# Kernel optimization log

Measured on AMD Instinct MI355X. Metric: run time of the kernel, lower is better.

The kernel has to match this reference:

```python
import jax, jax.numpy as jnp
import numpy as np

NUM_ITERATIONS = 3


def squash(s, axis):
    # s: capsule vectors; squash along `axis` (capsule dim)
    mag_sq = jnp.sum(s * s, axis=axis, keepdims=True)
    mag = jnp.sqrt(mag_sq)
    return mag_sq / (1.0 + mag_sq) * (s / mag)


def setup_inputs() -> dict:
    key = jax.random.key(0)
    k1, k2 = jax.random.split(key)
    B, IN_SIZE, I = 256, 8, 1152   # batch, in_size, in_node_num
    N, O = 10, 16                  # num_node, node_size
    x = jax.random.normal(k1, (B, IN_SIZE, I), dtype=jnp.float32)
    W = jax.random.normal(k2, (1, I, N, O, IN_SIZE), dtype=jnp.float32)
    return {"x": x, "W": W}


def reference(x, W):
    # x: (B, in_size, I); W: (1, I, N, O, in_size)
    B = x.shape[0]
    I, N = W.shape[1], W.shape[2]
    xt = jnp.swapaxes(x, 1, 2)  # (B, I, in_size)
    # u_hat[b,i,n,o] = sum_k (0.03*W[0,i,n,o,k]) * x[b,i,k]
    u_hat = jnp.einsum('inok,bik->bino', W[0] * 0.03, xt)  # (B, I, N, O)
    b_ij = jnp.zeros((I, N), dtype=x.dtype)
    v_j = None
    for _ in range(NUM_ITERATIONS):
        c_ij = jax.nn.softmax(b_ij, axis=1)              # softmax over num_node
        s_j = jnp.einsum('in,bino->bno', c_ij, u_hat)    # (B, N, O)
        v_j = squash(s_j, axis=-1)                       # squash over node_size
        # agreement: u_hat . v_j, averaged over batch
        u_vj = jnp.einsum('bino,bno->bin', u_hat, v_j).mean(axis=0)  # (I, N)
        b_ij = b_ij + u_vj
    return v_j[:, :, :, None]  # (B, N, O, 1) == v_j.squeeze(1) in torch
```

## Files before the change

kernel.cpp:

```cpp
#include <hip/hip_runtime.h>

#define B_   256
#define I_   1152
#define N_   10
#define P_   9216
#define NO_  160
#define BIJS 12
#define NBLK 1280

typedef unsigned short u16;
typedef short s8v __attribute__((ext_vector_type(8)));
typedef float f4v __attribute__((ext_vector_type(4)));

__device__ inline float bf2f(u16 u){
  unsigned v = ((unsigned)u) << 16; float f; __builtin_memcpy(&f, &v, 4); return f;
}
__device__ inline u16 f2bf(float f){
  unsigned b; __builtin_memcpy(&b, &f, 4);
  b += 0x7fffu + ((b >> 16) & 1u);
  return (u16)(b >> 16);
}
__device__ inline float ald1(const float* p){
  unsigned u = __hip_atomic_load((const unsigned*)p,
      __ATOMIC_RELAXED, __HIP_MEMORY_SCOPE_AGENT);
  float f; __builtin_memcpy(&f, &u, 4); return f;
}
__device__ inline void ast1(float* p, float v){
  unsigned u; __builtin_memcpy(&u, &v, 4);
  __hip_atomic_store((unsigned*)p, u, __ATOMIC_RELAXED, __HIP_MEMORY_SCOPE_AGENT);
}

#define CIX(j) ((j) + (((j) >> 3) << 1))

__global__ __launch_bounds__(128) void k_prep(
    const float* __restrict__ x, const float* __restrict__ W,
    u16* __restrict__ xbp, u16* __restrict__ xpb, u16* __restrict__ Wt,
    float* __restrict__ bij, float* __restrict__ sA, int* __restrict__ bar){
  __shared__ union { u16 w[8][136]; float t[32][68]; } sm;
  int t = threadIdx.x, u = blockIdx.x;
  if (u < 1440){
    int q = u/9, ch = u - q*9;
    int n = q >> 4, o = q & 15;
    int i = ch*128 + t;
    const float* src = W + (size_t)i*1280 + n*128 + o*8;
    float4 a = *reinterpret_cast<const float4*>(src);
    float4 b = *reinterpret_cast<const float4*>(src + 4);
    float vv[8] = {a.x,a.y,a.z,a.w,b.x,b.y,b.z,b.w};
    #pragma unroll
    for (int k = 0; k < 8; ++k) sm.w[k][t] = f2bf(vv[k] * 0.03f);
    __syncthreads();
    int k = t >> 4, seg = t & 15;
    uint4 val = *reinterpret_cast<const uint4*>(&sm.w[k][seg*8]);
    *reinterpret_cast<uint4*>(Wt + (size_t)q*P_ + (size_t)k*I_ + ch*128 + seg*8) = val;
  } else if (u < 2592){
    int v = u - 1440;
    int tb = v/144, tp = v - tb*144;
    int b0 = tb*32, p0 = tp*64;
    #pragma unroll
    for (int pass = 0; pass < 2; ++pass){
      int vt = t + (pass << 7);
      int r = vt >> 3, c8 = (vt & 7)*8;
      const float* sp = x + (size_t)(b0 + r)*P_ + p0 + c8;
      float4 a = *reinterpret_cast<const float4*>(sp);
      float4 b = *reinterpret_cast<const float4*>(sp + 4);
      *reinterpret_cast<float4*>(&sm.t[r][c8]) = a;
      *reinterpret_cast<float4*>(&sm.t[r][c8+4]) = b;
      uint4 pk;
      pk.x = (unsigned)f2bf(a.x) | ((unsigned)f2bf(a.y) << 16);
      pk.y = (unsigned)f2bf(a.z) | ((unsigned)f2bf(a.w) << 16);
      pk.z = (unsigned)f2bf(b.x) | ((unsigned)f2bf(b.y) << 16);
      pk.w = (unsigned)f2bf(b.z) | ((unsigned)f2bf(b.w) << 16);
      *reinterpret_cast<uint4*>(xbp + (size_t)(b0 + r)*P_ + p0 + c8) = pk;
    }
    __syncthreads();
    #pragma unroll
    for (int pass = 0; pass < 2; ++pass){
      int vt = t + (pass << 7);
      int pc = vt >> 2, rb = (vt & 3)*8;
      uint4 pk;
      pk.x = (unsigned)f2bf(sm.t[rb+0][pc]) | ((unsigned)f2bf(sm.t[rb+1][pc]) << 16);
      pk.y = (unsigned)f2bf(sm.t[rb+2][pc]) | ((unsigned)f2bf(sm.t[rb+3][pc]) << 16);
      pk.z = (unsigned)f2bf(sm.t[rb+4][pc]) | ((unsigned)f2bf(sm.t[rb+5][pc]) << 16);
      pk.w = (unsigned)f2bf(sm.t[rb+6][pc]) | ((unsigned)f2bf(sm.t[rb+7][pc]) << 16);
      *reinterpret_cast<uint4*>(xpb + (size_t)(p0 + pc)*B_ + b0 + rb) = pk;
    }
  } else if (u < 2700){
    bij[(u - 2592)*128 + t] = 0.f;
  } else if (u < 3020){
    sA[(u - 2700)*128 + t] = 0.f;
  } else {
    for (int z = t; z < 4128; z += 128) bar[z] = 0;
  }
}

__device__ inline void gbar(int* bar, int bid, int ph){
  __syncthreads();
  if (threadIdx.x == 0){
    int li = bid & 63;
    if (__hip_atomic_fetch_add(bar + li*32, 1, __ATOMIC_RELAXED,
                               __HIP_MEMORY_SCOPE_AGENT) == ph*20 - 1){
      if (__hip_atomic_fetch_add(bar + 4096, 1, __ATOMIC_RELAXED,
                                 __HIP_MEMORY_SCOPE_AGENT) == ph*64 - 1){
        #pragma unroll
        for (int z = 0; z < 64; ++z)
          __hip_atomic_store(bar + 2048 + z*32, ph, __ATOMIC_RELAXED,
                             __HIP_MEMORY_SCOPE_AGENT);
      }
    }
    while (__hip_atomic_load(bar + 2048 + li*32, __ATOMIC_RELAXED,
                             __HIP_MEMORY_SCOPE_AGENT) < ph)
      __builtin_amdgcn_s_sleep(4);
  }
  __syncthreads();
}

union LdsU {
  struct { float c[720]; u16 Bt[16][592]; } S;
  u16 vl[32][264];
};

__device__ inline void phase_C(int t, int bid,
    const float* __restrict__ bij, float* __restrict__ cT)
{
  if (bid < 9){
    int j = bid*128 + t;
    const float* br = bij + (size_t)j*BIJS;
    f4v a; f4v b4; float2 c2;
    asm volatile(
      "global_load_dwordx4 %0, %3, off sc0 sc1\n\t"
      "global_load_dwordx4 %1, %3, off offset:16 sc0 sc1\n\t"
      "global_load_dwordx2 %2, %3, off offset:32 sc0 sc1\n\t"
      "s_waitcnt vmcnt(0)"
      : "=&v"(a), "=&v"(b4), "=&v"(c2)
      : "v"(br) : "memory");
    float l[10] = {a[0],a[1],a[2],a[3],b4[0],b4[1],b4[2],b4[3],c2.x,c2.y};
    float mx = l[0];
    #pragma unroll
    for (int k = 1; k < 10; ++k) mx = fmaxf(mx, l[k]);
    float e[10]; float se = 0.f;
    #pragma unroll
    for (int k = 0; k < 10; ++k){ e[k] = __expf(l[k]-mx); se += e[k]; }
    float inv = 1.0f / se;
    #pragma unroll
    for (int k = 0; k < 10; ++k) ast1(&cT[k*I_ + j], e[k]*inv);
  }
}

__device__ inline void phase_S(int t, int bid,
    const u16* __restrict__ xbp, const u16* __restrict__ Wt,
    const float* __restrict__ cT, float* __restrict__ s_cur,
    float* __restrict__ s_zero, LdsU* lds)
{
  int kc = (bid & 7)*2 + ((bid >> 3) & 1);
  int g2 = bid >> 4;
  int n = g2 % 10, bx2 = g2 / 10;
  if (s_zero && t < 32) ast1(&s_zero[bid*32 + t], 0.f);
  int i0 = (kc & 1)*576;

  const float* cp = cT + (size_t)n*I_ + i0;
  {
    float4 v = *reinterpret_cast<const float4*>(cp + 4*t);
    int d = CIX(4*t);
    lds->S.c[d] = v.x; lds->S.c[d+1] = v.y; lds->S.c[d+2] = v.z; lds->S.c[d+3] = v.w;
    if (t < 16){
      float4 w = *reinterpret_cast<const float4*>(cp + 512 + 4*t);
      int d2 = CIX(512 + 4*t);
      lds->S.c[d2] = w.x; lds->S.c[d2+1] = w.y; lds->S.c[d2+2] = w.z; lds->S.c[d2+3] = w.w;
    }
  }
  __syncthreads();

  #pragma unroll
  for (int s9 = 0; s9 < 9; ++s9){
    int uu = t + s9*128;
    int r = uu / 72, m = uu - r*72;
    uint4 w = *reinterpret_cast<const uint4*>(Wt + (size_t)(n*16 + r)*P_ + kc*576 + m*8);
    const float* cc = &lds->S.c[10*m];
    float2 ca = *reinterpret_cast<const float2*>(cc);
    float2 cb = *reinterpret_cast<const float2*>(cc + 2);
    float2 cd = *reinterpret_cast<const float2*>(cc + 4);
    float2 ce = *reinterpret_cast<const float2*>(cc + 6);
    uint4 rr;
    rr.x = (unsigned)f2bf(bf2f(w.x & 0xffff)*ca.x) | ((unsigned)f2bf(bf2f(w.x >> 16)*ca.y) << 16);
    rr.y = (unsigned)f2bf(bf2f(w.y & 0xffff)*cb.x) | ((unsigned)f2bf(bf2f(w.y >> 16)*cb.y) << 16);
    rr.z = (unsigned)f2bf(bf2f(w.z & 0xffff)*cd.x) | ((unsigned)f2bf(bf2f(w.z >> 16)*cd.y) << 16);
    rr.w = (unsigned)f2bf(bf2f(w.w & 0xffff)*ce.x) | ((unsigned)f2bf(bf2f(w.w >> 16)*ce.y) << 16);
    *reinterpret_cast<uint4*>(&lds->S.Bt[r][m*8]) = rr;
  }
  __syncthreads();

  int wid = t >> 6, l = t & 63, lo = l & 15, quad = l >> 4;
  int b0 = bx2*32 + wid*16;
  const s8v* ap = reinterpret_cast<const s8v*>(xbp + (size_t)(b0 + lo)*P_ + kc*576 + quad*8);
  f4v acc0 = {0.f,0.f,0.f,0.f}, acc1 = {0.f,0.f,0.f,0.f};
  #pragma unroll
  for (int s = 0; s < 9; ++s){
    s8v a0 = ap[8*s];
    s8v b0v = *reinterpret_cast<const s8v*>(&lds->S.Bt[lo][quad*8 + 64*s]);
    s8v a1 = ap[8*s + 4];
    s8v b1v = *reinterpret_cast<const s8v*>(&lds->S.Bt[lo][quad*8 + 64*s + 32]);
    acc0 = __builtin_amdgcn_mfma_f32_16x16x32_bf16(a0, b0v, acc0, 0, 0, 0);
    acc1 = __builtin_amdgcn_mfma_f32_16x16x32_bf16(a1, b1v, acc1, 0, 0, 0);
  }
  f4v acc = acc0 + acc1;
  int r0 = quad << 2;
  #pragma unroll
  for (int r = 0; r < 4; ++r)
    atomicAdd(&s_cur[(size_t)(b0 + r0 + r)*NO_ + n*16 + lo], acc[r]);
}

__device__ inline void phase_G(int t, int bid,
    const u16* __restrict__ xpb, const float* __restrict__ s,
    const u16* __restrict__ Wt, float* __restrict__ bij, LdsU* lds)
{
  int qp = bid >> 8;
  #pragma unroll
  for (int h = 0; h < 2; ++h){
    int b = t + (h << 7);
    #pragma unroll
    for (int nn = 0; nn < 2; ++nn){
      const float* sr = s + (size_t)b*NO_ + (qp*2 + nn)*16;
      float4 s0 = *reinterpret_cast<const float4*>(sr);
      float4 s1 = *reinterpret_cast<const float4*>(sr + 4);
      float4 s2 = *reinterpret_cast<const float4*>(sr + 8);
      float4 s3 = *reinterpret_cast<const float4*>(sr + 12);
      float sq = s0.x*s0.x+s0.y*s0.y+s0.z*s0.z+s0.w*s0.w
               + s1.x*s1.x+s1.y*s1.y+s1.z*s1.z+s1.w*s1.w
               + s2.x*s2.x+s2.y*s2.y+s2.z*s2.z+s2.w*s2.w
               + s3.x*s3.x+s3.y*s3.y+s3.z*s3.z+s3.w*s3.w;
      float scale = sqrtf(sq) / (1.0f + sq);
      float sv[16] = {s0.x,s0.y,s0.z,s0.w,s1.x,s1.y,s1.z,s1.w,
                      s2.x,s2.y,s2.z,s2.w,s3.x,s3.y,s3.z,s3.w};
      #pragma unroll
      for (int o = 0; o < 16; ++o)
        lds->vl[nn*16 + o][b] = f2bf(sv[o] * scale);
    }
  }
  __syncthreads();

  int wv = t >> 6, l = t & 63, lo = l & 15, quad = l >> 4;
  int idx = (139*(bid & 255)) & 255;
  for (int u = idx*2 + wv; u < 576; u += 512){
    int p0 = u << 4;
    const s8v* ap = reinterpret_cast<const s8v*>(xpb + (size_t)(p0 + lo)*B_ + quad*8);
    f4v acc0 = {0.f,0.f,0.f,0.f}, acc1 = {0.f,0.f,0.f,0.f};
    #pragma unroll
    for (int st = 0; st < 8; ++st){
      s8v a  = ap[4*st];
      s8v b0 = *reinterpret_cast<const s8v*>(&lds->vl[lo]     [st*32 + quad*8]);
      s8v b1 = *reinterpret_cast<const s8v*>(&lds->vl[16 + lo][st*32 + quad*8]);
      acc0 = __builtin_amdgcn_mfma_f32_16x16x32_bf16(a, b0, acc0, 0, 0, 0);
      acc1 = __builtin_amdgcn_mfma_f32_16x16x32_bf16(a, b1, acc1, 0, 0, 0);
    }
    int ib = p0 % 1152;
    #pragma unroll
    for (int sb = 0; sb < 2; ++sb){
      f4v acc = sb ? acc1 : acc0;
      int n = qp*2 + sb;
      const u16* wp = Wt + (size_t)(n*16 + lo)*P_ + p0 + (quad << 2);
      ushort4 w4 = *reinterpret_cast<const ushort4*>(wp);
      float v0 = acc[0]*bf2f(w4.x), v1 = acc[1]*bf2f(w4.y);
      float v2 = acc[2]*bf2f(w4.z), v3 = acc[3]*bf2f(w4.w);
      #pragma unroll
      for (int m = 8; m >= 1; m >>= 1){
        v0 += __shfl_xor(v0, m, 16);
        v1 += __shfl_xor(v1, m, 16);
        v2 += __shfl_xor(v2, m, 16);
        v3 += __shfl_xor(v3, m, 16);
      }
      if (lo == 0){
        int i = ib + (quad << 2);
        atomicAdd(&bij[(size_t)(i+0)*BIJS + n], v0 * (1.f/256.f));
        atomicAdd(&bij[(size_t)(i+1)*BIJS + n], v1 * (1.f/256.f));
        atomicAdd(&bij[(size_t)(i+2)*BIJS + n], v2 * (1.f/256.f));
        atomicAdd(&bij[(size_t)(i+3)*BIJS + n], v3 * (1.f/256.f));
      }
    }
  }
}

__global__ __launch_bounds__(128, 3) void k_route(
    const u16* __restrict__ xbp, const u16* __restrict__ xpb,
    const u16* __restrict__ Wt, float* __restrict__ bij,
    float* __restrict__ cTa, float* __restrict__ cTb,
    float* __restrict__ sA, float* __restrict__ sB,
    float* __restrict__ out, int* __restrict__ bar)
{
  __shared__ LdsU lds;
  int t = threadIdx.x, bid = blockIdx.x;

  {
    int kc = (bid & 7)*2 + ((bid >> 3) & 1);
    int g2 = bid >> 4;
    int n = g2 % 10, bx2 = g2 / 10;
    if (t < 32) ast1(&sB[bid*32 + t], 0.f);
    int wid = t >> 6, l = t & 63, lo = l & 15, quad = l >> 4;
    int b0 = bx2*32 + wid*16;
    const s8v* ap = reinterpret_cast<const s8v*>(xbp + (size_t)(b0 + lo)*P_ + kc*576 + quad*8);
    const s8v* bp = reinterpret_cast<const s8v*>(Wt  + (size_t)(n*16 + lo)*P_ + kc*576 + quad*8);
    f4v acc0 = {0.f,0.f,0.f,0.f}, acc1 = {0.f,0.f,0.f,0.f};
    #pragma unroll
    for (int s = 0; s < 9; ++s){
      acc0 = __builtin_amdgcn_mfma_f32_16x16x32_bf16(ap[8*s],     bp[8*s],     acc0, 0, 0, 0);
      acc1 = __builtin_amdgcn_mfma_f32_16x16x32_bf16(ap[8*s + 4], bp[8*s + 4], acc1, 0, 0, 0);
    }
    f4v acc = acc0 + acc1;
    int r0 = quad << 2;
    #pragma unroll
    for (int r = 0; r < 4; ++r)
      atomicAdd(&sA[(size_t)(b0 + r0 + r)*NO_ + n*16 + lo], acc[r] * 0.1f);
  }
  gbar(bar, bid, 1);

  phase_G(t, bid, xpb, sA, Wt, bij, &lds);
  gbar(bar, bid, 2);

  phase_C(t, bid, bij, cTa);
  gbar(bar, bid, 3);

  phase_S(t, bid, xbp, Wt, cTa, sB, sA, &lds);
  gbar(bar, bid, 4);

  phase_G(t, bid, xpb, sB, Wt, bij, &lds);
  gbar(bar, bid, 5);

  phase_C(t, bid, bij, cTb);
  gbar(bar, bid, 6);

  phase_S(t, bid, xbp, Wt, cTb, sA, nullptr, &lds);
  gbar(bar, bid, 7);

  if (bid < 320){
    int o = t & 15, rl = t >> 4;
    int rowid = bid*8 + rl;
    int b = rowid / 10, n = rowid - b*10;
    size_t idx = (size_t)b*NO_ + n*16 + o;
    float sv = ald1(&sA[idx]);
    float sq = sv * sv;
    #pragma unroll
    for (int m = 8; m >= 1; m >>= 1) sq += __shfl_xor(sq, m, 16);
    out[idx] = sv * sqrtf(sq) / (1.0f + sq);
  }
}

extern "C" void kernel_launch(void* const* d_in, const int* in_sizes, int n_in,
                              void* d_out, int out_size, void* d_ws, size_t ws_size,
                              hipStream_t stream){
  (void)in_sizes; (void)n_in; (void)out_size; (void)ws_size;
  const float* x = (const float*)d_in[0];
  const float* W = (const float*)d_in[1];
  float* out = (float*)d_out;

  float* sA  = (float*)d_ws;
  float* sB  = sA + 40960;
  float* bij = sB + 40960;
  float* cTa = bij + 13824;
  float* cTb = cTa + 11520;
  u16* xbp = (u16*)(cTb + 11520);
  u16* xpb = xbp + 2359296;
  u16* Wt  = xpb + 2359296;
  int* bar = (int*)(Wt + 1474560);

  k_prep <<<3021, 128, 0, stream>>>(x, W, xbp, xpb, Wt, bij, sA, bar);
  k_route<<<NBLK, 128, 0, stream>>>(xbp, xpb, Wt, bij, cTa, cTb, sA, sB, out, bar);
}
```

Before: 141.3 us.

## Fuse agreement and softmax phases, halve grid, drop two grid barriers

Reworks the persistent routing kernel. Squash/v computation is done once by ten dedicated blocks into a global bf16 buffer, signalled through a counter instead of being recomputed in every block. The agreement reduction is repartitioned so each of 72 blocks owns 16 input capsules, accumulates b_ij in LDS and registers, and applies the softmax locally. This removes the global b_ij atomics and the separate softmax phase plus its grid barriers. The grid is halved to 640 blocks with twice the work per block in the S phases, which trades fewer barrier participants for less parallelism in the G phase, where only 72 blocks do the matmul work.

```diff
diff --git a/kernel.cpp b/kernel.cpp
--- a/kernel.cpp
+++ b/kernel.cpp
@@ -5,8 +5,7 @@
 #define N_   10
 #define P_   9216
 #define NO_  160
-#define BIJS 12
-#define NBLK 1280
+#define NBLK 640
 
 typedef unsigned short u16;
 typedef short s8v __attribute__((ext_vector_type(8)));
@@ -20,6 +19,12 @@
   b += 0x7fffu + ((b >> 16) & 1u);
   return (u16)(b >> 16);
 }
+__device__ inline void ald2(const float* p, float& a, float& b){
+  unsigned long long q = __hip_atomic_load((const unsigned long long*)p,
+      __ATOMIC_RELAXED, __HIP_MEMORY_SCOPE_AGENT);
+  unsigned lo = (unsigned)q, hi = (unsigned)(q >> 32);
+  __builtin_memcpy(&a, &lo, 4); __builtin_memcpy(&b, &hi, 4);
+}
 __device__ inline float ald1(const float* p){
   unsigned u = __hip_atomic_load((const unsigned*)p,
       __ATOMIC_RELAXED, __HIP_MEMORY_SCOPE_AGENT);
@@ -29,13 +34,16 @@
   unsigned u; __builtin_memcpy(&u, &v, 4);
   __hip_atomic_store((unsigned*)p, u, __ATOMIC_RELAXED, __HIP_MEMORY_SCOPE_AGENT);
 }
+__device__ inline void astu(unsigned* p, unsigned v){
+  __hip_atomic_store(p, v, __ATOMIC_RELAXED, __HIP_MEMORY_SCOPE_AGENT);
+}
 
 #define CIX(j) ((j) + (((j) >> 3) << 1))
 
 __global__ __launch_bounds__(128) void k_prep(
     const float* __restrict__ x, const float* __restrict__ W,
     u16* __restrict__ xbp, u16* __restrict__ xpb, u16* __restrict__ Wt,
-    float* __restrict__ bij, float* __restrict__ sA, int* __restrict__ bar){
+    float* __restrict__ sA, int* __restrict__ bar){
   __shared__ union { u16 w[8][136]; float t[32][68]; } sm;
   int t = threadIdx.x, u = blockIdx.x;
   if (u < 1440){
@@ -84,10 +92,8 @@
       pk.w = (unsigned)f2bf(sm.t[rb+6][pc]) | ((unsigned)f2bf(sm.t[rb+7][pc]) << 16);
       *reinterpret_cast<uint4*>(xpb + (size_t)(p0 + pc)*B_ + b0 + rb) = pk;
     }
-  } else if (u < 2700){
-    bij[(u - 2592)*128 + t] = 0.f;
-  } else if (u < 3020){
-    sA[(u - 2700)*128 + t] = 0.f;
+  } else if (u < 2912){
+    sA[(u - 2592)*128 + t] = 0.f;
   } else {
     for (int z = t; z < 4128; z += 128) bar[z] = 0;
   }
@@ -98,7 +104,7 @@
   if (threadIdx.x == 0){
     int li = bid & 63;
     if (__hip_atomic_fetch_add(bar + li*32, 1, __ATOMIC_RELAXED,
-                               __HIP_MEMORY_SCOPE_AGENT) == ph*20 - 1){
+                               __HIP_MEMORY_SCOPE_AGENT) == ph*10 - 1){
       if (__hip_atomic_fetch_add(bar + 4096, 1, __ATOMIC_RELAXED,
                                  __HIP_MEMORY_SCOPE_AGENT) == ph*64 - 1){
         #pragma unroll
@@ -116,33 +122,107 @@
 
 union LdsU {
   struct { float c[720]; u16 Bt[16][592]; } S;
-  u16 vl[32][264];
+  struct { float bijL[16][10]; } G;
 };
 
-__device__ inline void phase_C(int t, int bid,
-    const float* __restrict__ bij, float* __restrict__ cT)
+__device__ inline void phase_VG(int t, int bid,
+    const u16* __restrict__ xpb, const u16* __restrict__ Wt,
+    const float* __restrict__ s, u16* __restrict__ vbt,
+    float* __restrict__ cT, int* __restrict__ bar, int vthr,
+    float* bijr, LdsU* lds)
 {
-  if (bid < 9){
-    int j = bid*128 + t;
-    const float* br = bij + (size_t)j*BIJS;
-    f4v a; f4v b4; float2 c2;
-    asm volatile(
-      "global_load_dwordx4 %0, %3, off sc0 sc1\n\t"
-      "global_load_dwordx4 %1, %3, off offset:16 sc0 sc1\n\t"
-      "global_load_dwordx2 %2, %3, off offset:32 sc0 sc1\n\t"
-      "s_waitcnt vmcnt(0)"
-      : "=&v"(a), "=&v"(b4), "=&v"(c2)
-      : "v"(br) : "memory");
-    float l[10] = {a[0],a[1],a[2],a[3],b4[0],b4[1],b4[2],b4[3],c2.x,c2.y};
-    float mx = l[0];
-    #pragma unroll
-    for (int k = 1; k < 10; ++k) mx = fmaxf(mx, l[k]);
-    float e[10]; float se = 0.f;
-    #pragma unroll
-    for (int k = 0; k < 10; ++k){ e[k] = __expf(l[k]-mx); se += e[k]; }
-    float inv = 1.0f / se;
-    #pragma unroll
-    for (int k = 0; k < 10; ++k) ast1(&cT[k*I_ + j], e[k]*inv);
+  if (bid >= 72 && bid < 82){
+    int n = bid - 72, bp = t, b0 = bp*2;
+    const float* s0p = s + (size_t)b0*NO_ + n*16;
+    const float* s1p = s0p + NO_;
+    float v0[16], v1[16];
+    #pragma unroll
+    for (int k = 0; k < 8; ++k){
+      ald2(s0p + 2*k, v0[2*k], v0[2*k+1]);
+      ald2(s1p + 2*k, v1[2*k], v1[2*k+1]);
+    }
+    float sq0 = 0.f, sq1 = 0.f;
+    #pragma unroll
+    for (int o = 0; o < 16; ++o){ sq0 += v0[o]*v0[o]; sq1 += v1[o]*v1[o]; }
+    float sc0 = sqrtf(sq0)/(1.0f + sq0), sc1 = sqrtf(sq1)/(1.0f + sq1);
+    unsigned* vb32 = reinterpret_cast<unsigned*>(vbt);
+    #pragma unroll
+    for (int o = 0; o < 16; ++o){
+      unsigned pk = (unsigned)f2bf(v0[o]*sc0) | ((unsigned)f2bf(v1[o]*sc1) << 16);
+      astu(&vb32[(n*16 + o)*128 + bp], pk);
+    }
+    __syncthreads();
+    if (t == 0)
+      __hip_atomic_fetch_add(bar + 4100, 1, __ATOMIC_RELAXED, __HIP_MEMORY_SCOPE_AGENT);
+  } else if (bid < 72){
+    for (int z = t; z < 160; z += 128)
+      reinterpret_cast<float*>(lds->G.bijL)[z] = 0.f;
+    if (t == 0){
+      while (__hip_atomic_load(bar + 4100, __ATOMIC_RELAXED,
+                               __HIP_MEMORY_SCOPE_AGENT) < vthr)
+        __builtin_amdgcn_s_sleep(2);
+    }
+    __syncthreads();
+    int wv = t >> 6, l = t & 63, lo = l & 15, quad = l >> 4;
+    int i0 = bid*16;
+    #pragma unroll
+    for (int kk = 0; kk < 4; ++kk){
+      int k = wv*4 + kk;
+      int p0 = k*1152 + i0;
+      const s8v* ap = reinterpret_cast<const s8v*>(xpb + (size_t)(p0 + lo)*B_ + quad*8);
+      #pragma unroll
+      for (int np = 0; np < 5; ++np){
+        int n0 = np*2;
+        const s8v* b0p = reinterpret_cast<const s8v*>(vbt + (size_t)(n0*16 + lo)*B_ + quad*8);
+        const s8v* b1p = reinterpret_cast<const s8v*>(vbt + (size_t)((n0+1)*16 + lo)*B_ + quad*8);
+        f4v acc0 = {0.f,0.f,0.f,0.f}, acc1 = {0.f,0.f,0.f,0.f};
+        #pragma unroll
+        for (int st = 0; st < 8; ++st){
+          s8v a = ap[4*st];
+          acc0 = __builtin_amdgcn_mfma_f32_16x16x32_bf16(a, b0p[4*st], acc0, 0, 0, 0);
+          acc1 = __builtin_amdgcn_mfma_f32_16x16x32_bf16(a, b1p[4*st], acc1, 0, 0, 0);
+        }
+        #pragma unroll
+        for (int sb = 0; sb < 2; ++sb){
+          f4v acc = sb ? acc1 : acc0;
+          int n = n0 + sb;
+          ushort4 w4 = *reinterpret_cast<const ushort4*>(
+              Wt + (size_t)(n*16 + lo)*P_ + p0 + quad*4);
+          float v0 = acc[0]*bf2f(w4.x), v1 = acc[1]*bf2f(w4.y);
+          float v2 = acc[2]*bf2f(w4.z), v3 = acc[3]*bf2f(w4.w);
+          #pragma unroll
+          for (int m = 8; m >= 1; m >>= 1){
+            v0 += __shfl_xor(v0, m, 16);
+            v1 += __shfl_xor(v1, m, 16);
+            v2 += __shfl_xor(v2, m, 16);
+            v3 += __shfl_xor(v3, m, 16);
+          }
+          if (lo == 0){
+            int r0 = quad*4;
+            atomicAdd(&lds->G.bijL[r0+0][n], v0 * (1.f/256.f));
+            atomicAdd(&lds->G.bijL[r0+1][n], v1 * (1.f/256.f));
+            atomicAdd(&lds->G.bijL[r0+2][n], v2 * (1.f/256.f));
+            atomicAdd(&lds->G.bijL[r0+3][n], v3 * (1.f/256.f));
+          }
+        }
+      }
+    }
+    __syncthreads();
+    if (t < 16){
+      float e[10]; float mx = -1e30f;
+      #pragma unroll
+      for (int j = 0; j < 10; ++j){
+        bijr[j] += lds->G.bijL[t][j];
+        mx = fmaxf(mx, bijr[j]);
+      }
+      float se = 0.f;
+      #pragma unroll
+      for (int j = 0; j < 10; ++j){ e[j] = __expf(bijr[j] - mx); se += e[j]; }
+      float inv = 1.0f / se;
+      #pragma unroll
+      for (int j = 0; j < 10; ++j)
+        ast1(&cT[(size_t)j*I_ + i0 + t], e[j] * inv);
+    }
   }
 }
 
@@ -151,56 +231,57 @@
     const float* __restrict__ cT, float* __restrict__ s_cur,
     float* __restrict__ s_zero, LdsU* lds)
 {
-  int kc = (bid & 7)*2 + ((bid >> 3) & 1);
-  int g2 = bid >> 4;
-  int n = g2 % 10, bx2 = g2 / 10;
-  if (s_zero && t < 32) ast1(&s_zero[bid*32 + t], 0.f);
-  int i0 = (kc & 1)*576;
-
-  const float* cp = cT + (size_t)n*I_ + i0;
-  {
-    float4 v = *reinterpret_cast<const float4*>(cp + 4*t);
-    int d = CIX(4*t);
-    lds->S.c[d] = v.x; lds->S.c[d+1] = v.y; lds->S.c[d+2] = v.z; lds->S.c[d+3] = v.w;
-    if (t < 16){
-      float4 w = *reinterpret_cast<const float4*>(cp + 512 + 4*t);
-      int d2 = CIX(512 + 4*t);
-      lds->S.c[d2] = w.x; lds->S.c[d2+1] = w.y; lds->S.c[d2+2] = w.z; lds->S.c[d2+3] = w.w;
-    }
-  }
-  __syncthreads();
-
-  #pragma unroll
-  for (int s9 = 0; s9 < 9; ++s9){
-    int uu = t + s9*128;
-    int r = uu / 72, m = uu - r*72;
-    uint4 w = *reinterpret_cast<const uint4*>(Wt + (size_t)(n*16 + r)*P_ + kc*576 + m*8);
-    const float* cc = &lds->S.c[10*m];
-    float2 ca = *reinterpret_cast<const float2*>(cc);
-    float2 cb = *reinterpret_cast<const float2*>(cc + 2);
-    float2 cd = *reinterpret_cast<const float2*>(cc + 4);
-    float2 ce = *reinterpret_cast<const float2*>(cc + 6);
-    uint4 rr;
-    rr.x = (unsigned)f2bf(bf2f(w.x & 0xffff)*ca.x) | ((unsigned)f2bf(bf2f(w.x >> 16)*ca.y) << 16);
-    rr.y = (unsigned)f2bf(bf2f(w.y & 0xffff)*cb.x) | ((unsigned)f2bf(bf2f(w.y >> 16)*cb.y) << 16);
-    rr.z = (unsigned)f2bf(bf2f(w.z & 0xffff)*cd.x) | ((unsigned)f2bf(bf2f(w.z >> 16)*cd.y) << 16);
-    rr.w = (unsigned)f2bf(bf2f(w.w & 0xffff)*ce.x) | ((unsigned)f2bf(bf2f(w.w >> 16)*ce.y) << 16);
-    *reinterpret_cast<uint4*>(&lds->S.Bt[r][m*8]) = rr;
-  }
-  __syncthreads();
-
+  int kc = bid & 7, rest = bid >> 3;
+  int n = rest % 10, bx2 = rest / 10;
+  if (s_zero && t < 64) ast1(&s_zero[bid*64 + t], 0.f);
   int wid = t >> 6, l = t & 63, lo = l & 15, quad = l >> 4;
   int b0 = bx2*32 + wid*16;
-  const s8v* ap = reinterpret_cast<const s8v*>(xbp + (size_t)(b0 + lo)*P_ + kc*576 + quad*8);
   f4v acc0 = {0.f,0.f,0.f,0.f}, acc1 = {0.f,0.f,0.f,0.f};
+
   #pragma unroll
-  for (int s = 0; s < 9; ++s){
-    s8v a0 = ap[8*s];
-    s8v b0v = *reinterpret_cast<const s8v*>(&lds->S.Bt[lo][quad*8 + 64*s]);
-    s8v a1 = ap[8*s + 4];
-    s8v b1v = *reinterpret_cast<const s8v*>(&lds->S.Bt[lo][quad*8 + 64*s + 32]);
-    acc0 = __builtin_amdgcn_mfma_f32_16x16x32_bf16(a0, b0v, acc0, 0, 0, 0);
-    acc1 = __builtin_amdgcn_mfma_f32_16x16x32_bf16(a1, b1v, acc1, 0, 0, 0);
+  for (int h2 = 0; h2 < 2; ++h2){
+    int off = kc*1152 + h2*576;
+    const float* cp = cT + (size_t)n*I_ + h2*576;
+    __syncthreads();
+    {
+      float4 v = *reinterpret_cast<const float4*>(cp + 4*t);
+      int d = CIX(4*t);
+      lds->S.c[d] = v.x; lds->S.c[d+1] = v.y; lds->S.c[d+2] = v.z; lds->S.c[d+3] = v.w;
+      if (t < 16){
+        float4 w = *reinterpret_cast<const float4*>(cp + 512 + 4*t);
+        int d2 = CIX(512 + 4*t);
+        lds->S.c[d2] = w.x; lds->S.c[d2+1] = w.y; lds->S.c[d2+2] = w.z; lds->S.c[d2+3] = w.w;
+      }
+    }
+    __syncthreads();
+    #pragma unroll
+    for (int s9 = 0; s9 < 9; ++s9){
+      int uu = t + s9*128;
+      int r = uu / 72, m = uu - r*72;
+      uint4 w = *reinterpret_cast<const uint4*>(Wt + (size_t)(n*16 + r)*P_ + off + m*8);
+      const float* cc = &lds->S.c[10*m];
+      float2 ca = *reinterpret_cast<const float2*>(cc);
+      float2 cb = *reinterpret_cast<const float2*>(cc + 2);
+      float2 cd = *reinterpret_cast<const float2*>(cc + 4);
+      float2 ce = *reinterpret_cast<const float2*>(cc + 6);
+      uint4 rr;
+      rr.x = (unsigned)f2bf(bf2f(w.x & 0xffff)*ca.x) | ((unsigned)f2bf(bf2f(w.x >> 16)*ca.y) << 16);
+      rr.y = (unsigned)f2bf(bf2f(w.y & 0xffff)*cb.x) | ((unsigned)f2bf(bf2f(w.y >> 16)*cb.y) << 16);
+      rr.z = (unsigned)f2bf(bf2f(w.z & 0xffff)*cd.x) | ((unsigned)f2bf(bf2f(w.z >> 16)*cd.y) << 16);
+      rr.w = (unsigned)f2bf(bf2f(w.w & 0xffff)*ce.x) | ((unsigned)f2bf(bf2f(w.w >> 16)*ce.y) << 16);
+      *reinterpret_cast<uint4*>(&lds->S.Bt[r][m*8]) = rr;
+    }
+    __syncthreads();
+    const s8v* ap = reinterpret_cast<const s8v*>(xbp + (size_t)(b0 + lo)*P_ + off + quad*8);
+    #pragma unroll
+    for (int s = 0; s < 9; ++s){
+      s8v a0 = ap[8*s];
+      s8v b0v = *reinterpret_cast<const s8v*>(&lds->S.Bt[lo][quad*8 + 64*s]);
+      s8v a1 = ap[8*s + 4];
+      s8v b1v = *reinterpret_cast<const s8v*>(&lds->S.Bt[lo][quad*8 + 64*s + 32]);
+      acc0 = __builtin_amdgcn_mfma_f32_16x16x32_bf16(a0, b0v, acc0, 0, 0, 0);
+      acc1 = __builtin_amdgcn_mfma_f32_16x16x32_bf16(a1, b1v, acc1, 0, 0, 0);
+    }
   }
   f4v acc = acc0 + acc1;
   int r0 = quad << 2;
@@ -209,98 +290,31 @@
     atomicAdd(&s_cur[(size_t)(b0 + r0 + r)*NO_ + n*16 + lo], acc[r]);
 }
 
-__device__ inline void phase_G(int t, int bid,
-    const u16* __restrict__ xpb, const float* __restrict__ s,
-    const u16* __restrict__ Wt, float* __restrict__ bij, LdsU* lds)
-{
-  int qp = bid >> 8;
-  #pragma unroll
-  for (int h = 0; h < 2; ++h){
-    int b = t + (h << 7);
-    #pragma unroll
-    for (int nn = 0; nn < 2; ++nn){
-      const float* sr = s + (size_t)b*NO_ + (qp*2 + nn)*16;
-      float4 s0 = *reinterpret_cast<const float4*>(sr);
-      float4 s1 = *reinterpret_cast<const float4*>(sr + 4);
-      float4 s2 = *reinterpret_cast<const float4*>(sr + 8);
-      float4 s3 = *reinterpret_cast<const float4*>(sr + 12);
-      float sq = s0.x*s0.x+s0.y*s0.y+s0.z*s0.z+s0.w*s0.w
-               + s1.x*s1.x+s1.y*s1.y+s1.z*s1.z+s1.w*s1.w
-               + s2.x*s2.x+s2.y*s2.y+s2.z*s2.z+s2.w*s2.w
-               + s3.x*s3.x+s3.y*s3.y+s3.z*s3.z+s3.w*s3.w;
-      float scale = sqrtf(sq) / (1.0f + sq);
-      float sv[16] = {s0.x,s0.y,s0.z,s0.w,s1.x,s1.y,s1.z,s1.w,
-                      s2.x,s2.y,s2.z,s2.w,s3.x,s3.y,s3.z,s3.w};
-      #pragma unroll
-      for (int o = 0; o < 16; ++o)
-        lds->vl[nn*16 + o][b] = f2bf(sv[o] * scale);
-    }
-  }
-  __syncthreads();
-
-  int wv = t >> 6, l = t & 63, lo = l & 15, quad = l >> 4;
-  int idx = (139*(bid & 255)) & 255;
-  for (int u = idx*2 + wv; u < 576; u += 512){
-    int p0 = u << 4;
-    const s8v* ap = reinterpret_cast<const s8v*>(xpb + (size_t)(p0 + lo)*B_ + quad*8);
-    f4v acc0 = {0.f,0.f,0.f,0.f}, acc1 = {0.f,0.f,0.f,0.f};
-    #pragma unroll
-    for (int st = 0; st < 8; ++st){
-      s8v a  = ap[4*st];
-      s8v b0 = *reinterpret_cast<const s8v*>(&lds->vl[lo]     [st*32 + quad*8]);
-      s8v b1 = *reinterpret_cast<const s8v*>(&lds->vl[16 + lo][st*32 + quad*8]);
-      acc0 = __builtin_amdgcn_mfma_f32_16x16x32_bf16(a, b0, acc0, 0, 0, 0);
-      acc1 = __builtin_amdgcn_mfma_f32_16x16x32_bf16(a, b1, acc1, 0, 0, 0);
-    }
-    int ib = p0 % 1152;
-    #pragma unroll
-    for (int sb = 0; sb < 2; ++sb){
-      f4v acc = sb ? acc1 : acc0;
-      int n = qp*2 + sb;
-      const u16* wp = Wt + (size_t)(n*16 + lo)*P_ + p0 + (quad << 2);
-      ushort4 w4 = *reinterpret_cast<const ushort4*>(wp);
-      float v0 = acc[0]*bf2f(w4.x), v1 = acc[1]*bf2f(w4.y);
-      float v2 = acc[2]*bf2f(w4.z), v3 = acc[3]*bf2f(w4.w);
-      #pragma unroll
-      for (int m = 8; m >= 1; m >>= 1){
-        v0 += __shfl_xor(v0, m, 16);
-        v1 += __shfl_xor(v1, m, 16);
-        v2 += __shfl_xor(v2, m, 16);
-        v3 += __shfl_xor(v3, m, 16);
-      }
-      if (lo == 0){
-        int i = ib + (quad << 2);
-        atomicAdd(&bij[(size_t)(i+0)*BIJS + n], v0 * (1.f/256.f));
-        atomicAdd(&bij[(size_t)(i+1)*BIJS + n], v1 * (1.f/256.f));
-        atomicAdd(&bij[(size_t)(i+2)*BIJS + n], v2 * (1.f/256.f));
-        atomicAdd(&bij[(size_t)(i+3)*BIJS + n], v3 * (1.f/256.f));
-      }
-    }
-  }
-}
-
-__global__ __launch_bounds__(128, 3) void k_route(
+__global__ __launch_bounds__(128, 2) void k_route(
     const u16* __restrict__ xbp, const u16* __restrict__ xpb,
-    const u16* __restrict__ Wt, float* __restrict__ bij,
+    const u16* __restrict__ Wt,
     float* __restrict__ cTa, float* __restrict__ cTb,
+    u16* __restrict__ vbtA, u16* __restrict__ vbtB,
     float* __restrict__ sA, float* __restrict__ sB,
     float* __restrict__ out, int* __restrict__ bar)
 {
   __shared__ LdsU lds;
   int t = threadIdx.x, bid = blockIdx.x;
+  float bijr[10];
+  #pragma unroll
+  for (int j = 0; j < 10; ++j) bijr[j] = 0.f;
 
   {
-    int kc = (bid & 7)*2 + ((bid >> 3) & 1);
-    int g2 = bid >> 4;
-    int n = g2 % 10, bx2 = g2 / 10;
-    if (t < 32) ast1(&sB[bid*32 + t], 0.f);
+    int kc = bid & 7, rest = bid >> 3;
+    int n = rest % 10, bx2 = rest / 10;
+    if (t < 64) ast1(&sB[bid*64 + t], 0.f);
     int wid = t >> 6, l = t & 63, lo = l & 15, quad = l >> 4;
     int b0 = bx2*32 + wid*16;
-    const s8v* ap = reinterpret_cast<const s8v*>(xbp + (size_t)(b0 + lo)*P_ + kc*576 + quad*8);
-    const s8v* bp = reinterpret_cast<const s8v*>(Wt  + (size_t)(n*16 + lo)*P_ + kc*576 + quad*8);
+    const s8v* ap = reinterpret_cast<const s8v*>(xbp + (size_t)(b0 + lo)*P_ + kc*1152 + quad*8);
+    const s8v* bp = reinterpret_cast<const s8v*>(Wt  + (size_t)(n*16 + lo)*P_ + kc*1152 + quad*8);
     f4v acc0 = {0.f,0.f,0.f,0.f}, acc1 = {0.f,0.f,0.f,0.f};
     #pragma unroll
-    for (int s = 0; s < 9; ++s){
+    for (int s = 0; s < 18; ++s){
       acc0 = __builtin_amdgcn_mfma_f32_16x16x32_bf16(ap[8*s],     bp[8*s],     acc0, 0, 0, 0);
       acc1 = __builtin_amdgcn_mfma_f32_16x16x32_bf16(ap[8*s + 4], bp[8*s + 4], acc1, 0, 0, 0);
     }
@@ -312,23 +326,17 @@
   }
   gbar(bar, bid, 1);
 
-  phase_G(t, bid, xpb, sA, Wt, bij, &lds);
+  phase_VG(t, bid, xpb, Wt, sA, vbtA, cTa, bar, 10, bijr, &lds);
   gbar(bar, bid, 2);
 
-  phase_C(t, bid, bij, cTa);
+  phase_S(t, bid, xbp, Wt, cTa, sB, sA, &lds);
   gbar(bar, bid, 3);
 
-  phase_S(t, bid, xbp, Wt, cTa, sB, sA, &lds);
+  phase_VG(t, bid, xpb, Wt, sB, vbtB, cTb, bar, 20, bijr, &lds);
   gbar(bar, bid, 4);
 
-  phase_G(t, bid, xpb, sB, Wt, bij, &lds);
+  phase_S(t, bid, xbp, Wt, cTb, sA, nullptr, &lds);
   gbar(bar, bid, 5);
-
-  phase_C(t, bid, bij, cTb);
-  gbar(bar, bid, 6);
-
-  phase_S(t, bid, xbp, Wt, cTb, sA, nullptr, &lds);
-  gbar(bar, bid, 7);
 
   if (bid < 320){
     int o = t & 15, rl = t >> 4;
@@ -353,14 +361,16 @@
 
   float* sA  = (float*)d_ws;
   float* sB  = sA + 40960;
-  float* bij = sB + 40960;
-  float* cTa = bij + 13824;
+  float* cTa = sB + 40960;
   float* cTb = cTa + 11520;
-  u16* xbp = (u16*)(cTb + 11520);
+  u16* vbtA = (u16*)(cTb + 11520);
+  u16* vbtB = vbtA + 40960;
+  u16* xbp = vbtB + 40960;
   u16* xpb = xbp + 2359296;
   u16* Wt  = xpb + 2359296;
   int* bar = (int*)(Wt + 1474560);
 
-  k_prep <<<3021, 128, 0, stream>>>(x, W, xbp, xpb, Wt, bij, sA, bar);
-  k_route<<<NBLK, 128, 0, stream>>>(xbp, xpb, Wt, bij, cTa, cTb, sA, sB, out, bar);
-}
+  k_prep <<<2913, 128, 0, stream>>>(x, W, xbp, xpb, Wt, sA, bar);
+  k_route<<<NBLK, 128, 0, stream>>>(xbp, xpb, Wt, cTa, cTb, vbtA, vbtB,
+                                    sA, sB, out, bar);
+}
```

After: 221.9 us. 1.57x slower.

## Replace full grid barriers after softmax with a counter wait and prefetch W

Applied to the files above, without the earlier changes.

Drops the grid-wide barriers that followed each softmax phase. Instead, the 9 blocks that compute softmax bump a global counter, and every block spins on that counter before starting the S phase. Each block also loads its W slice into registers once before the first barrier and reuses it in both S phases, which removes repeated global loads. The trade-off is higher register pressure from the 9 uint4 values, a new spin-wait that all 1280 blocks poll, and a dependency on the counter at bar+4100 being zeroed between launches.

```diff
diff --git a/kernel.cpp b/kernel.cpp
--- a/kernel.cpp
+++ b/kernel.cpp
@@ -120,7 +120,8 @@
 };
 
 __device__ inline void phase_C(int t, int bid,
-    const float* __restrict__ bij, float* __restrict__ cT)
+    const float* __restrict__ bij, float* __restrict__ cT,
+    int* __restrict__ bar, int target)
 {
   if (bid < 9){
     int j = bid*128 + t;
@@ -143,17 +144,24 @@
     float inv = 1.0f / se;
     #pragma unroll
     for (int k = 0; k < 10; ++k) ast1(&cT[k*I_ + j], e[k]*inv);
-  }
-}
-
-__device__ inline void phase_S(int t, int bid,
-    const u16* __restrict__ xbp, const u16* __restrict__ Wt,
+    __syncthreads();
+    if (t == 0)
+      __hip_atomic_fetch_add(bar + 4100, 1, __ATOMIC_RELAXED,
+                             __HIP_MEMORY_SCOPE_AGENT);
+  }
+  if (t == 0){
+    while (__hip_atomic_load(bar + 4100, __ATOMIC_RELAXED,
+                             __HIP_MEMORY_SCOPE_AGENT) < target)
+      __builtin_amdgcn_s_sleep(2);
+  }
+  __syncthreads();
+}
+
+__device__ inline void phase_S(int t, int bid, int kc, int n, int bx2,
+    const u16* __restrict__ xbp, const uint4* wpre,
     const float* __restrict__ cT, float* __restrict__ s_cur,
     float* __restrict__ s_zero, LdsU* lds)
 {
-  int kc = (bid & 7)*2 + ((bid >> 3) & 1);
-  int g2 = bid >> 4;
-  int n = g2 % 10, bx2 = g2 / 10;
   if (s_zero && t < 32) ast1(&s_zero[bid*32 + t], 0.f);
   int i0 = (kc & 1)*576;
 
@@ -174,7 +182,7 @@
   for (int s9 = 0; s9 < 9; ++s9){
     int uu = t + s9*128;
     int r = uu / 72, m = uu - r*72;
-    uint4 w = *reinterpret_cast<const uint4*>(Wt + (size_t)(n*16 + r)*P_ + kc*576 + m*8);
+    uint4 w = wpre[s9];
     const float* cc = &lds->S.c[10*m];
     float2 ca = *reinterpret_cast<const float2*>(cc);
     float2 cb = *reinterpret_cast<const float2*>(cc + 2);
@@ -288,11 +296,11 @@
 {
   __shared__ LdsU lds;
   int t = threadIdx.x, bid = blockIdx.x;
+  int kc = (bid & 7)*2 + ((bid >> 3) & 1);
+  int g2 = bid >> 4;
+  int n = g2 % 10, bx2 = g2 / 10;
 
   {
-    int kc = (bid & 7)*2 + ((bid >> 3) & 1);
-    int g2 = bid >> 4;
-    int n = g2 % 10, bx2 = g2 / 10;
     if (t < 32) ast1(&sB[bid*32 + t], 0.f);
     int wid = t >> 6, l = t & 63, lo = l & 15, quad = l >> 4;
     int b0 = bx2*32 + wid*16;
@@ -313,28 +321,32 @@
   gbar(bar, bid, 1);
 
   phase_G(t, bid, xpb, sA, Wt, bij, &lds);
+  uint4 wpre[9];
+  #pragma unroll
+  for (int s9 = 0; s9 < 9; ++s9){
+    int uu = t + s9*128;
+    int r = uu / 72, m = uu - r*72;
+    wpre[s9] = *reinterpret_cast<const uint4*>(
+        Wt + (size_t)(n*16 + r)*P_ + kc*576 + m*8);
+  }
   gbar(bar, bid, 2);
 
-  phase_C(t, bid, bij, cTa);
+  phase_C(t, bid, bij, cTa, bar, 9);
+  phase_S(t, bid, kc, n, bx2, xbp, wpre, cTa, sB, sA, &lds);
   gbar(bar, bid, 3);
 
-  phase_S(t, bid, xbp, Wt, cTa, sB, sA, &lds);
+  phase_G(t, bid, xpb, sB, Wt, bij, &lds);
   gbar(bar, bid, 4);
 
-  phase_G(t, bid, xpb, sB, Wt, bij, &lds);
+  phase_C(t, bid, bij, cTb, bar, 18);
+  phase_S(t, bid, kc, n, bx2, xbp, wpre, cTb, sA, nullptr, &lds);
   gbar(bar, bid, 5);
-
-  phase_C(t, bid, bij, cTb);
-  gbar(bar, bid, 6);
-
-  phase_S(t, bid, xbp, Wt, cTb, sA, nullptr, &lds);
-  gbar(bar, bid, 7);
 
   if (bid < 320){
     int o = t & 15, rl = t >> 4;
     int rowid = bid*8 + rl;
-    int b = rowid / 10, n = rowid - b*10;
-    size_t idx = (size_t)b*NO_ + n*16 + o;
+    int b = rowid / 10, nn = rowid - b*10;
+    size_t idx = (size_t)b*NO_ + nn*16 + o;
     float sv = ald1(&sA[idx]);
     float sq = sv * sv;
     #pragma unroll
```

New measurement: 151.9 us. 7.5% more time.
